# Optimization experiments

Hardware: AMD Instinct MI355X
Metric: run time of the kernel (lower is better)

Reference implementation:

```python
import jax, jax.numpy as jnp
from jax import lax
import numpy as np

B, L, W = 32, 128, 16
CHAR_VOCAB, CHAR_EMBED = 100, 64
NUM_FILTERS, KERNEL = 128, 3
WORD_VOCAB, WORD_EMBED = 50000, 256
EMBED = NUM_FILTERS + WORD_EMBED  # 384
HIDDEN = 512
OUT_SIZE = 512
NUM_CLASSES = 17


def setup_inputs() -> dict:
    key = jax.random.key(0)
    ks = jax.random.split(key, 16)
    s = 0.05
    char_emb = jax.random.normal(ks[0], (CHAR_VOCAB, CHAR_EMBED), jnp.float32) * s
    char_emb = char_emb.at[0].set(0.0)  # padding_idx=0
    word_emb = jax.random.normal(ks[1], (WORD_VOCAB, WORD_EMBED), jnp.float32) * s
    conv_w = jax.random.normal(ks[2], (NUM_FILTERS, CHAR_EMBED, KERNEL), jnp.float32) * s
    conv_b = jnp.zeros((NUM_FILTERS,), jnp.float32)
    G = 4 * HIDDEN
    w_ih_f = jax.random.normal(ks[3], (G, EMBED), jnp.float32) * s
    w_hh_f = jax.random.normal(ks[4], (G, HIDDEN), jnp.float32) * s
    b_f = jax.random.normal(ks[5], (G,), jnp.float32) * s
    w_ih_b = jax.random.normal(ks[6], (G, EMBED), jnp.float32) * s
    w_hh_b = jax.random.normal(ks[7], (G, HIDDEN), jnp.float32) * s
    b_b = jax.random.normal(ks[8], (G,), jnp.float32) * s
    w1 = jax.random.normal(ks[9], (OUT_SIZE, 2 * HIDDEN), jnp.float32) * s
    b1 = jnp.zeros((OUT_SIZE,), jnp.float32)
    w2 = jax.random.normal(ks[10], (NUM_CLASSES, OUT_SIZE), jnp.float32) * s
    b2 = jnp.zeros((NUM_CLASSES,), jnp.float32)
    word_ids = jax.random.randint(ks[11], (B, L), 0, WORD_VOCAB, jnp.int32)
    char_ids = jax.random.randint(ks[12], (B, L, W), 0, CHAR_VOCAB, jnp.int32)
    mask = jnp.ones((B, L), jnp.bool_)
    return dict(word_ids=word_ids, char_ids=char_ids, mask=mask,
                char_emb=char_emb, word_emb=word_emb, conv_w=conv_w, conv_b=conv_b,
                w_ih_f=w_ih_f, w_hh_f=w_hh_f, b_f=b_f,
                w_ih_b=w_ih_b, w_hh_b=w_hh_b, b_b=b_b,
                w1=w1, b1=b1, w2=w2, b2=b2)


def _lstm_scan(xs, w_ih, w_hh, b):
    # xs: [L, B, E] -> hs: [L, B, H]; PyTorch gate order i,f,g,o
    H = w_hh.shape[1]
    gates_x = jnp.einsum('lbe,ge->lbg', xs, w_ih) + b  # precompute input projection

    def step(carry, gx):
        h, c = carry
        gates = gx + h @ w_hh.T
        i, f, g, o = jnp.split(gates, 4, axis=-1)
        c = jax.nn.sigmoid(f) * c + jax.nn.sigmoid(i) * jnp.tanh(g)
        h = jax.nn.sigmoid(o) * jnp.tanh(c)
        return (h, c), h

    nB = xs.shape[1]
    init = (jnp.zeros((nB, H), xs.dtype), jnp.zeros((nB, H), xs.dtype))
    _, hs = lax.scan(step, init, gates_x)
    return hs


def reference(word_ids, char_ids, mask, char_emb, word_emb, conv_w, conv_b,
              w_ih_f, w_hh_f, b_f, w_ih_b, w_hh_b, b_b, w1, b1, w2, b2):
    Bb, Ll, Ww = char_ids.shape
    # char CNN
    ce = char_emb[char_ids.reshape(Bb * Ll, Ww)]         # [BL, W, Cc]
    ce = ce.transpose(0, 2, 1)                           # [BL, Cc, W]
    pad = conv_w.shape[2] // 2
    y = lax.conv_general_dilated(ce, conv_w, (1,), [(pad, pad)],
                                 dimension_numbers=('NCH', 'OIH', 'NCH'))
    y = jax.nn.relu(y + conv_b[None, :, None])           # [BL, F, W]
    char_x = y.max(axis=2).reshape(Bb, Ll, -1)           # [B, L, F]
    # word embedding + concat
    x = jnp.concatenate([char_x, word_emb[word_ids]], axis=-1)  # [B, L, E]
    # bidirectional LSTM (dropout is identity in eval)
    xs = x.transpose(1, 0, 2)                            # [L, B, E]
    hf = _lstm_scan(xs, w_ih_f, w_hh_f, b_f)
    hb = _lstm_scan(xs[::-1], w_ih_b, w_hh_b, b_b)[::-1]
    h = jnp.concatenate([hf, hb], axis=-1).transpose(1, 0, 2)  # [B, L, 2H]
    # head: Linear -> ELU -> Linear
    z = jax.nn.elu(h @ w1.T + b1)
    return z @ w2.T + b2                                 # [B, L, num_classes]
```

## Files before the change

kernel.cpp:

```cpp
#include <hip/hip_runtime.h>
#include <math.h>

#define B_   32
#define L_   128
#define W_   16
#define CE_  64
#define NF_  128
#define WE_  256
#define E_   384
#define H_   512
#define G4_  2048
#define O1_  512
#define NC_  17
#define LSTM_BLOCKS 64
#define AGENT_SC __HIP_MEMORY_SCOPE_AGENT

typedef __attribute__((ext_vector_type(4))) float f32x4;
typedef _Float16 half8 __attribute__((ext_vector_type(8)));
typedef _Float16 half4 __attribute__((ext_vector_type(4)));

__device__ inline half8 cvt8(float4 a, float4 b) {
    half8 r;
    r[0] = (_Float16)a.x; r[1] = (_Float16)a.y;
    r[2] = (_Float16)a.z; r[3] = (_Float16)a.w;
    r[4] = (_Float16)b.x; r[5] = (_Float16)b.y;
    r[6] = (_Float16)b.z; r[7] = (_Float16)b.w;
    return r;
}

__global__ __launch_bounds__(256) void conv_transpose_k(
    const float* __restrict__ cw, float* __restrict__ cwT)
{
    int i = blockIdx.x * 256 + threadIdx.x;
    int f = i / 192;
    int rem = i - f * 192;
    int c = rem / 3;
    int k = rem - c * 3;
    cwT[(c * 3 + k) * NF_ + f] = cw[i];
}

__global__ __launch_bounds__(64) void embed_cnn(
    const int* __restrict__ word_ids, const int* __restrict__ char_ids,
    const float* __restrict__ char_emb, const float* __restrict__ word_emb,
    const float* __restrict__ cwT, const float* __restrict__ conv_b,
    _Float16* __restrict__ x_h)
{
    __shared__ float ce[CE_][20];
    __shared__ int ids[W_];
    int bl = blockIdx.x;
    int tid = threadIdx.x;

    if (tid < W_) ids[tid] = char_ids[bl * W_ + tid];
    ce[tid][0] = 0.f;
    ce[tid][17] = 0.f;
    __syncthreads();

    for (int i = tid; i < W_ * CE_; i += 64) {
        int w = i >> 6, c = i & 63;
        ce[c][w + 1] = char_emb[ids[w] * CE_ + c];
    }
    __syncthreads();

    int f0 = tid, f1 = tid + 64;
    float acc0[W_], acc1[W_];
#pragma unroll
    for (int w = 0; w < W_; w++) { acc0[w] = 0.f; acc1[w] = 0.f; }

    for (int c = 0; c < CE_; c++) {
        float win[18];
        float4 v0 = *(const float4*)&ce[c][0];
        float4 v1 = *(const float4*)&ce[c][4];
        float4 v2 = *(const float4*)&ce[c][8];
        float4 v3 = *(const float4*)&ce[c][12];
        win[0]=v0.x; win[1]=v0.y; win[2]=v0.z; win[3]=v0.w;
        win[4]=v1.x; win[5]=v1.y; win[6]=v1.z; win[7]=v1.w;
        win[8]=v2.x; win[9]=v2.y; win[10]=v2.z; win[11]=v2.w;
        win[12]=v3.x; win[13]=v3.y; win[14]=v3.z; win[15]=v3.w;
        win[16] = ce[c][16];
        win[17] = ce[c][17];
        const float* wp = cwT + c * 3 * NF_;
        float k00 = wp[f0], k01 = wp[NF_ + f0], k02 = wp[2 * NF_ + f0];
        float k10 = wp[f1], k11 = wp[NF_ + f1], k12 = wp[2 * NF_ + f1];
#pragma unroll
        for (int w = 0; w < W_; w++) {
            acc0[w] += win[w] * k00 + win[w + 1] * k01 + win[w + 2] * k02;
            acc1[w] += win[w] * k10 + win[w + 1] * k11 + win[w + 2] * k12;
        }
    }
    float m0 = acc0[0], m1 = acc1[0];
#pragma unroll
    for (int w = 1; w < W_; w++) { m0 = fmaxf(m0, acc0[w]); m1 = fmaxf(m1, acc1[w]); }
    m0 = fmaxf(0.f, m0 + conv_b[f0]);
    m1 = fmaxf(0.f, m1 + conv_b[f1]);
    x_h[bl * E_ + f0] = (_Float16)m0;
    x_h[bl * E_ + f1] = (_Float16)m1;

    int wid = word_ids[bl];
    float4 wv = *(const float4*)&word_emb[wid * WE_ + tid * 4];
    half4 h;
    h[0] = (_Float16)wv.x; h[1] = (_Float16)wv.y;
    h[2] = (_Float16)wv.z; h[3] = (_Float16)wv.w;
    *(half4*)&x_h[bl * E_ + NF_ + tid * 4] = h;
}

__global__ __launch_bounds__(256) void gemm_f16(
    const _Float16* __restrict__ A, const float* __restrict__ Wt,
    const float* __restrict__ bias, void* __restrict__ C,
    int N, int K, int mode, int act, int fp16out)
{
    __shared__ _Float16 As[64 * 32];
    __shared__ _Float16 Bs[64 * 32];
    int tid = threadIdx.x;
    int bm = blockIdx.x * 64;
    int bn = blockIdx.y * 64;
    int l = tid & 63;
    int mt = tid >> 6;
    int lr = l & 15, lk = l >> 4;

    int srow = tid >> 2, skq = (tid & 3) << 3;
    int sbyteA = ((srow * 64 + skq * 2) ^ ((srow & 7) << 4));

    f32x4 d[4] = {{0.f,0.f,0.f,0.f},{0.f,0.f,0.f,0.f},
                  {0.f,0.f,0.f,0.f},{0.f,0.f,0.f,0.f}};

    for (int kt = 0; kt < K; kt += 32) {
        half8 av = *(const half8*)&A[(size_t)(bm + srow) * K + kt + skq];
        const float* wp = &Wt[(size_t)(bn + srow) * K + kt + skq];
        float4 w0 = *(const float4*)wp;
        float4 w1 = *(const float4*)(wp + 4);
        *(half8*)((char*)As + sbyteA) = av;
        *(half8*)((char*)Bs + sbyteA) = cvt8(w0, w1);
        __syncthreads();

        int arow = mt * 16 + lr;
        half8 af = *(const half8*)((char*)As +
                     ((arow * 64 + lk * 16) ^ ((arow & 7) << 4)));
#pragma unroll
        for (int nt = 0; nt < 4; nt++) {
            int brow = nt * 16 + lr;
            half8 bf = *(const half8*)((char*)Bs +
                         ((brow * 64 + lk * 16) ^ ((brow & 7) << 4)));
            d[nt] = __builtin_amdgcn_mfma_f32_16x16x32_f16(af, bf, d[nt], 0, 0, 0);
        }
        __syncthreads();
    }

#pragma unroll
    for (int nt = 0; nt < 4; nt++) {
        int n = bn + nt * 16 + lr;
        float bv = bias[n];
#pragma unroll
        for (int r = 0; r < 4; r++) {
            int m = bm + mt * 16 + lk * 4 + r;
            int orow;
            if (mode == 0) orow = m;
            else {
                int bb = m >> 7, ll = m & 127;
                if (mode == 2) ll = 127 - ll;
                orow = ll * B_ + bb;
            }
            float v = d[nt][r] + bv;
            if (act) v = v > 0.f ? v : expm1f(v);
            if (fp16out) ((_Float16*)C)[(size_t)orow * N + n] = (_Float16)v;
            else         ((float*)C)[(size_t)orow * N + n] = v;
        }
    }
}

__global__ __launch_bounds__(256) void gemm_bias_act(
    const float* __restrict__ A, const float* __restrict__ Wt,
    const float* __restrict__ bias, float* __restrict__ C,
    int M, int N, int K)
{
    __shared__ float As[16][68];
    __shared__ float Bs[16][68];
    int tid = threadIdx.x;
    int bm = blockIdx.x * 64;
    int bn = blockIdx.y * 64;
    int tx = tid & 15, ty = tid >> 4;
    int r = tid >> 2, kq = (tid & 3) << 2;
    float acc[4][4] = {};

    for (int kt = 0; kt < K; kt += 16) {
        float4 av = *(const float4*)&A[(bm + r) * K + kt + kq];
        As[kq + 0][r] = av.x; As[kq + 1][r] = av.y;
        As[kq + 2][r] = av.z; As[kq + 3][r] = av.w;
        int n = bn + r;
        float4 wv = make_float4(0.f, 0.f, 0.f, 0.f);
        if (n < N) wv = *(const float4*)&Wt[n * K + kt + kq];
        Bs[kq + 0][r] = wv.x; Bs[kq + 1][r] = wv.y;
        Bs[kq + 2][r] = wv.z; Bs[kq + 3][r] = wv.w;
        __syncthreads();
#pragma unroll
        for (int k = 0; k < 16; k++) {
            float4 a = *(const float4*)&As[k][ty << 2];
            float4 b = *(const float4*)&Bs[k][tx << 2];
            acc[0][0] += a.x * b.x; acc[0][1] += a.x * b.y;
            acc[0][2] += a.x * b.z; acc[0][3] += a.x * b.w;
            acc[1][0] += a.y * b.x; acc[1][1] += a.y * b.y;
            acc[1][2] += a.y * b.z; acc[1][3] += a.y * b.w;
            acc[2][0] += a.z * b.x; acc[2][1] += a.z * b.y;
            acc[2][2] += a.z * b.z; acc[2][3] += a.z * b.w;
            acc[3][0] += a.w * b.x; acc[3][1] += a.w * b.y;
            acc[3][2] += a.w * b.z; acc[3][3] += a.w * b.w;
        }
        __syncthreads();
    }

#pragma unroll
    for (int ii = 0; ii < 4; ii++) {
        int m = bm + (ty << 2) + ii;
#pragma unroll
        for (int jj = 0; jj < 4; jj++) {
            int n = bn + (tx << 2) + jj;
            if (n < N) C[m * N + n] = acc[ii][jj] + bias[n];
        }
    }
}

__global__ __launch_bounds__(256) void lstm_mfma2(
    const float* __restrict__ gxf, const float* __restrict__ gxb,
    const float* __restrict__ whh_f, const float* __restrict__ whh_b,
    unsigned int* __restrict__ hbuf,
    _Float16* __restrict__ hcat_h,
    unsigned int* __restrict__ flags)
{
    __shared__ unsigned int hlds[8192];
    __shared__ float gl[4 * 32 * 17];

    int bx = blockIdx.x;
    int dir = bx >> 5;
    int U0 = (bx & 31) * 16;
    int tid = threadIdx.x;
    int g = tid >> 6;
    int l = tid & 63;
    int lr = l & 15, lk = l >> 4;

    const float* gx = dir ? gxb : gxf;

    half8 afrag[16];
    {
        const float* wrow = (dir ? whh_b : whh_f)
                          + (size_t)(g * 512 + U0 + lr) * 512 + lk * 8;
#pragma unroll
        for (int ks = 0; ks < 16; ks++) {
            float4 a = *(const float4*)(wrow + ks * 32);
            float4 b = *(const float4*)(wrow + ks * 32 + 4);
            afrag[ks] = cvt8(a, b);
        }
    }

    int uu = tid & 15, ub = tid >> 4;
    float c0 = 0.f, c1 = 0.f;
    const unsigned int* dflags = flags + dir * 32;

    for (int t = 0; t < L_; t++) {
        if (t > 0) {
            unsigned tgt = (unsigned)t;
            int fi = tid & 31;
            while (__hip_atomic_load(&dflags[fi], __ATOMIC_RELAXED, AGENT_SC) < tgt)
                __builtin_amdgcn_s_sleep(1);
            __builtin_amdgcn_sched_barrier(0);
        }

        {
            const unsigned int* hsrc = hbuf + ((((t + 1) & 1) * 2 + dir) * (32 * 256));
            unsigned int tmp[32];
#pragma unroll
            for (int p = 0; p < 32; p++)
                tmp[p] = __hip_atomic_load(&hsrc[tid + p * 256],
                                           __ATOMIC_RELAXED, AGENT_SC);
#pragma unroll
            for (int p = 0; p < 32; p++) {
                int w = tid + p * 256;
                int byte = (w << 2);
                int row = w >> 8;
                hlds[(byte ^ ((row & 7) << 4)) >> 2] = tmp[p];
            }
        }

        float gxv0[4], gxv1[4];
        {
            const float* gxt = gx + (size_t)t * B_ * G4_;
#pragma unroll
            for (int gg = 0; gg < 4; gg++) {
                gxv0[gg] = gxt[ub * G4_ + gg * H_ + U0 + uu];
                gxv1[gg] = gxt[(ub + 16) * G4_ + gg * H_ + U0 + uu];
            }
        }
        __syncthreads();

        f32x4 d0 = {0.f, 0.f, 0.f, 0.f};
        f32x4 d1 = {0.f, 0.f, 0.f, 0.f};
        const char* hb = (const char*)hlds;
        int base0 = lr * 1024 + lk * 16;
        int base1 = (16 + lr) * 1024 + lk * 16;
        int sw0 = (lr & 7) << 4;
#pragma unroll
        for (int ks = 0; ks < 16; ks++) {
            half8 b0 = *(const half8*)(hb + ((base0 + ks * 64) ^ sw0));
            half8 b1 = *(const half8*)(hb + ((base1 + ks * 64) ^ sw0));
            d0 = __builtin_amdgcn_mfma_f32_16x16x32_f16(afrag[ks], b0, d0, 0, 0, 0);
            d1 = __builtin_amdgcn_mfma_f32_16x16x32_f16(afrag[ks], b1, d1, 0, 0, 0);
        }
#pragma unroll
        for (int r = 0; r < 4; r++) {
            gl[(g * 32 + lr) * 17 + lk * 4 + r]      = d0[r];
            gl[(g * 32 + 16 + lr) * 17 + lk * 4 + r] = d1[r];
        }
        __syncthreads();

        {
            float ga0[4], ga1[4];
#pragma unroll
            for (int gg = 0; gg < 4; gg++) {
                ga0[gg] = gl[(gg * 32 + ub) * 17 + uu] + gxv0[gg];
                ga1[gg] = gl[(gg * 32 + ub + 16) * 17 + uu] + gxv1[gg];
            }
            float i0 = 1.f / (1.f + expf(-ga0[0]));
            float f0_ = 1.f / (1.f + expf(-ga0[1]));
            float g0 = tanhf(ga0[2]);
            float o0 = 1.f / (1.f + expf(-ga0[3]));
            c0 = f0_ * c0 + i0 * g0;
            float h0 = o0 * tanhf(c0);

            float i1 = 1.f / (1.f + expf(-ga1[0]));
            float f1_ = 1.f / (1.f + expf(-ga1[1]));
            float g1 = tanhf(ga1[2]);
            float o1 = 1.f / (1.f + expf(-ga1[3]));
            c1 = f1_ * c1 + i1 * g1;
            float h1 = o1 * tanhf(c1);

            int j = U0 + uu;
            int ll = dir ? (L_ - 1 - t) : t;
            hcat_h[((size_t)ub * L_ + ll) * (2 * H_) + dir * H_ + j]        = (_Float16)h0;
            hcat_h[((size_t)(ub + 16) * L_ + ll) * (2 * H_) + dir * H_ + j] = (_Float16)h1;

            float h0n = __shfl_xor(h0, 1);
            float h1n = __shfl_xor(h1, 1);
            if ((uu & 1) == 0) {
                union { _Float16 h[2]; unsigned u; } p0, p1;
                p0.h[0] = (_Float16)h0; p0.h[1] = (_Float16)h0n;
                p1.h[0] = (_Float16)h1; p1.h[1] = (_Float16)h1n;
                unsigned int* hdst = hbuf + (((t & 1) * 2 + dir) * (32 * 256));
                int wj = (U0 + uu) >> 1;
                __hip_atomic_store(&hdst[ub * 256 + wj], p0.u,
                                   __ATOMIC_RELAXED, AGENT_SC);
                __hip_atomic_store(&hdst[(ub + 16) * 256 + wj], p1.u,
                                   __ATOMIC_RELAXED, AGENT_SC);
            }
        }

        __syncthreads();
        if (tid == 0)
            __hip_atomic_store((unsigned int*)&flags[bx], (unsigned)(t + 1),
                               __ATOMIC_RELAXED, AGENT_SC);
    }
}

extern "C" void kernel_launch(void* const* d_in, const int* in_sizes, int n_in,
                              void* d_out, int out_size, void* d_ws, size_t ws_size,
                              hipStream_t stream)
{
    const int*   word_ids = (const int*)d_in[0];
    const int*   char_ids = (const int*)d_in[1];
    const float* char_emb = (const float*)d_in[3];
    const float* word_emb = (const float*)d_in[4];
    const float* conv_w   = (const float*)d_in[5];
    const float* conv_b   = (const float*)d_in[6];
    const float* w_ih_f   = (const float*)d_in[7];
    const float* w_hh_f   = (const float*)d_in[8];
    const float* b_f      = (const float*)d_in[9];
    const float* w_ih_b   = (const float*)d_in[10];
    const float* w_hh_b   = (const float*)d_in[11];
    const float* b_b      = (const float*)d_in[12];
    const float* w1       = (const float*)d_in[13];
    const float* b1       = (const float*)d_in[14];
    const float* w2       = (const float*)d_in[15];
    const float* b2       = (const float*)d_in[16];
    float* out = (float*)d_out;
    float* ws  = (float*)d_ws;

    _Float16* x_h   = (_Float16*)(ws + 0);
    float* gxf  = ws + 786432;
    float* gxb  = ws + 9175040;
    _Float16* hcat_h = (_Float16*)(ws + 17563648);
    float* z    = ws + 19660800;
    unsigned int* hbuf = (unsigned int*)(ws + 21757952);
    float* cwT  = ws + 21823488;
    unsigned int* flags = (unsigned int*)(ws + 21848064);

    hipMemsetAsync(hbuf, 0, 2 * 2 * 32 * 256 * sizeof(unsigned int), stream);
    hipMemsetAsync(flags, 0, 64 * sizeof(unsigned int), stream);

    conv_transpose_k<<<96, 256, 0, stream>>>(conv_w, cwT);
    embed_cnn<<<4096, 64, 0, stream>>>(word_ids, char_ids, char_emb, word_emb,
                                       cwT, conv_b, x_h);

    dim3 g1(64, 32);
    gemm_f16<<<g1, 256, 0, stream>>>(x_h, w_ih_f, b_f, gxf, G4_, E_, 1, 0, 0);
    gemm_f16<<<g1, 256, 0, stream>>>(x_h, w_ih_b, b_b, gxb, G4_, E_, 2, 0, 0);

    {
        const float* a0 = gxf; const float* a1 = gxb;
        const float* a2 = w_hh_f; const float* a3 = w_hh_b;
        unsigned int* a4 = hbuf;
        _Float16* a5 = hcat_h;
        unsigned int* a6 = flags;
        void* args[] = { &a0, &a1, &a2, &a3, &a4, &a5, &a6 };
        hipLaunchCooperativeKernel((void*)lstm_mfma2, dim3(LSTM_BLOCKS), dim3(256),
                                   args, 0, stream);
    }

    dim3 g2(64, 8);
    gemm_f16<<<g2, 256, 0, stream>>>(hcat_h, w1, b1, z, O1_, 2 * H_, 0, 1, 0);
    dim3 g3(64, 1);
    gemm_bias_act<<<g3, 256, 0, stream>>>(z, w2, b2, out, 4096, NC_, O1_);
}
```

Before: 715.6 us.

## Read LSTM hidden state directly from global into MFMA fragments with counter barrier

The recurrent LSTM kernel no longer stages the hidden state through shared memory. Each wave loads its B fragments straight from global memory with sc1 loads, which drops one __syncthreads per step. The 32 per-block flags that were polled are replaced by one atomic counter per direction, so each step waits on a single address, and the final-step signal is skipped. Sigmoid and tanh now use fast __expf formulations. In exchange, every wave issues redundant global loads, coherence depends on inline-asm cache bits, and the activations are slightly less accurate.

Measured after the change: 1.039 ms. 45.1% more time.

```diff
diff --git a/kernel.cpp b/kernel.cpp
--- a/kernel.cpp
+++ b/kernel.cpp
@@ -27,6 +27,22 @@
     r[6] = (_Float16)b.z; r[7] = (_Float16)b.w;
     return r;
 }
+
+__device__ inline unsigned int ld_u32_sc1(const unsigned int* p) {
+    unsigned int v;
+    asm volatile("global_load_dword %0, %1, off sc1\n\ts_waitcnt vmcnt(0)"
+                 : "=v"(v) : "v"(p) : "memory");
+    return v;
+}
+__device__ inline half8 ld_b128_sc1(const void* p) {
+    half8 v;
+    asm volatile("global_load_dwordx4 %0, %1, off sc1"
+                 : "=v"(v) : "v"(p) : "memory");
+    return v;
+}
+
+__device__ inline float sigm_f(float x) { return 1.f / (1.f + __expf(-x)); }
+__device__ inline float tanh_f(float x) { return 2.f / (1.f + __expf(-2.f * x)) - 1.f; }
 
 __global__ __launch_bounds__(256) void conv_transpose_k(
     const float* __restrict__ cw, float* __restrict__ cwT)
@@ -218,14 +234,13 @@
     }
 }
 
-__global__ __launch_bounds__(256) void lstm_mfma2(
+__global__ __launch_bounds__(256) void lstm_mfma3(
     const float* __restrict__ gxf, const float* __restrict__ gxb,
     const float* __restrict__ whh_f, const float* __restrict__ whh_b,
     unsigned int* __restrict__ hbuf,
     _Float16* __restrict__ hcat_h,
     unsigned int* __restrict__ flags)
 {
-    __shared__ unsigned int hlds[8192];
     __shared__ float gl[4 * 32 * 17];
 
     int bx = blockIdx.x;
@@ -252,33 +267,9 @@
 
     int uu = tid & 15, ub = tid >> 4;
     float c0 = 0.f, c1 = 0.f;
-    const unsigned int* dflags = flags + dir * 32;
+    unsigned int* cntp = flags + dir * 32;
 
     for (int t = 0; t < L_; t++) {
-        if (t > 0) {
-            unsigned tgt = (unsigned)t;
-            int fi = tid & 31;
-            while (__hip_atomic_load(&dflags[fi], __ATOMIC_RELAXED, AGENT_SC) < tgt)
-                __builtin_amdgcn_s_sleep(1);
-            __builtin_amdgcn_sched_barrier(0);
-        }
-
-        {
-            const unsigned int* hsrc = hbuf + ((((t + 1) & 1) * 2 + dir) * (32 * 256));
-            unsigned int tmp[32];
-#pragma unroll
-            for (int p = 0; p < 32; p++)
-                tmp[p] = __hip_atomic_load(&hsrc[tid + p * 256],
-                                           __ATOMIC_RELAXED, AGENT_SC);
-#pragma unroll
-            for (int p = 0; p < 32; p++) {
-                int w = tid + p * 256;
-                int byte = (w << 2);
-                int row = w >> 8;
-                hlds[(byte ^ ((row & 7) << 4)) >> 2] = tmp[p];
-            }
-        }
-
         float gxv0[4], gxv1[4];
         {
             const float* gxt = gx + (size_t)t * B_ * G4_;
@@ -288,20 +279,33 @@
                 gxv1[gg] = gxt[(ub + 16) * G4_ + gg * H_ + U0 + uu];
             }
         }
-        __syncthreads();
+
+        if (t > 0) {
+            unsigned tgt = (unsigned)(32 * t);
+            while (ld_u32_sc1(cntp) < tgt)
+                __builtin_amdgcn_s_sleep(1);
+            __builtin_amdgcn_sched_barrier(0);
+        }
+
+        const char* hsrc = (const char*)(hbuf
+                         + ((((t + 1) & 1) * 2 + dir) * (32 * 256)));
+        const char* hb0 = hsrc + lr * 1024 + lk * 16;
+        const char* hb1 = hb0 + 16 * 1024;
+        half8 fb0[16], fb1[16];
+#pragma unroll
+        for (int ks = 0; ks < 16; ks++) {
+            fb0[ks] = ld_b128_sc1(hb0 + ks * 64);
+            fb1[ks] = ld_b128_sc1(hb1 + ks * 64);
+        }
+        asm volatile("s_waitcnt vmcnt(0)" ::: "memory");
+        __builtin_amdgcn_sched_barrier(0);
 
         f32x4 d0 = {0.f, 0.f, 0.f, 0.f};
         f32x4 d1 = {0.f, 0.f, 0.f, 0.f};
-        const char* hb = (const char*)hlds;
-        int base0 = lr * 1024 + lk * 16;
-        int base1 = (16 + lr) * 1024 + lk * 16;
-        int sw0 = (lr & 7) << 4;
 #pragma unroll
         for (int ks = 0; ks < 16; ks++) {
-            half8 b0 = *(const half8*)(hb + ((base0 + ks * 64) ^ sw0));
-            half8 b1 = *(const half8*)(hb + ((base1 + ks * 64) ^ sw0));
-            d0 = __builtin_amdgcn_mfma_f32_16x16x32_f16(afrag[ks], b0, d0, 0, 0, 0);
-            d1 = __builtin_amdgcn_mfma_f32_16x16x32_f16(afrag[ks], b1, d1, 0, 0, 0);
+            d0 = __builtin_amdgcn_mfma_f32_16x16x32_f16(afrag[ks], fb0[ks], d0, 0, 0, 0);
+            d1 = __builtin_amdgcn_mfma_f32_16x16x32_f16(afrag[ks], fb1[ks], d1, 0, 0, 0);
         }
 #pragma unroll
         for (int r = 0; r < 4; r++) {
@@ -317,19 +321,19 @@
                 ga0[gg] = gl[(gg * 32 + ub) * 17 + uu] + gxv0[gg];
                 ga1[gg] = gl[(gg * 32 + ub + 16) * 17 + uu] + gxv1[gg];
             }
-            float i0 = 1.f / (1.f + expf(-ga0[0]));
-            float f0_ = 1.f / (1.f + expf(-ga0[1]));
-            float g0 = tanhf(ga0[2]);
-            float o0 = 1.f / (1.f + expf(-ga0[3]));
+            float i0 = sigm_f(ga0[0]);
+            float f0_ = sigm_f(ga0[1]);
+            float g0 = tanh_f(ga0[2]);
+            float o0 = sigm_f(ga0[3]);
             c0 = f0_ * c0 + i0 * g0;
-            float h0 = o0 * tanhf(c0);
-
-            float i1 = 1.f / (1.f + expf(-ga1[0]));
-            float f1_ = 1.f / (1.f + expf(-ga1[1]));
-            float g1 = tanhf(ga1[2]);
-            float o1 = 1.f / (1.f + expf(-ga1[3]));
+            float h0 = o0 * tanh_f(c0);
+
+            float i1 = sigm_f(ga1[0]);
+            float f1_ = sigm_f(ga1[1]);
+            float g1 = tanh_f(ga1[2]);
+            float o1 = sigm_f(ga1[3]);
             c1 = f1_ * c1 + i1 * g1;
-            float h1 = o1 * tanhf(c1);
+            float h1 = o1 * tanh_f(c1);
 
             int j = U0 + uu;
             int ll = dir ? (L_ - 1 - t) : t;
@@ -351,10 +355,11 @@
             }
         }
 
-        __syncthreads();
-        if (tid == 0)
-            __hip_atomic_store((unsigned int*)&flags[bx], (unsigned)(t + 1),
-                               __ATOMIC_RELAXED, AGENT_SC);
+        if (t < L_ - 1) {
+            __syncthreads();
+            if (tid == 0)
+                __hip_atomic_fetch_add(cntp, 1u, __ATOMIC_RELAXED, AGENT_SC);
+        }
     }
 }
 
@@ -408,7 +413,7 @@
         _Float16* a5 = hcat_h;
         unsigned int* a6 = flags;
         void* args[] = { &a0, &a1, &a2, &a3, &a4, &a5, &a6 };
-        hipLaunchCooperativeKernel((void*)lstm_mfma2, dim3(LSTM_BLOCKS), dim3(256),
+        hipLaunchCooperativeKernel((void*)lstm_mfma3, dim3(LSTM_BLOCKS), dim3(256),
                                    args, 0, stream);
     }
 
```
